# Performance work log

Hardware: AMD Instinct MI355X
Metric: run time of the kernel (lower is better)

Reference implementation:

```python
import jax, jax.numpy as jnp
import numpy as np

NUM_HEADS = 16
ROPE_BASE = 10000.0


def _rope_cos_sin(seq_len, head_dim, dtype):
    inv_freq = 1.0 / (ROPE_BASE ** (jnp.arange(0, head_dim, 2, dtype=jnp.float32) / head_dim))
    t = jnp.arange(seq_len, dtype=jnp.float32)
    freqs = t[:, None] * inv_freq[None, :]          # [S, hd/2]
    emb = jnp.concatenate([freqs, freqs], axis=-1)  # [S, hd]
    return jnp.cos(emb).astype(dtype), jnp.sin(emb).astype(dtype)


def _rotate_half(x):
    x1, x2 = jnp.split(x, 2, axis=-1)
    return jnp.concatenate([-x2, x1], axis=-1)


def setup_inputs() -> dict:
    key = jax.random.key(0)
    ks = jax.random.split(key, 5)
    B, S, D = 2, 2048, 2048
    x = jax.random.normal(ks[0], (B, S, D), dtype=jnp.float32)
    Wq = jax.random.normal(ks[1], (D, D), dtype=jnp.float32) * (D ** -0.5)
    Wk = jax.random.normal(ks[2], (D, D), dtype=jnp.float32) * (D ** -0.5)
    Wv = jax.random.normal(ks[3], (D, D), dtype=jnp.float32) * (D ** -0.5)
    Wo = jax.random.normal(ks[4], (D, D), dtype=jnp.float32) * (D ** -0.5)
    return {"x": x, "Wq": Wq, "Wk": Wk, "Wv": Wv, "Wo": Wo}


def reference(x, Wq, Wk, Wv, Wo):
    B, S, D = x.shape
    H = NUM_HEADS
    hd = D // H
    scale = hd ** -0.5
    # Linear(bias=False): y = x @ W.T ; reshape to [B, H, S, hd]
    def proj(W):
        return jnp.einsum('bsd,ed->bse', x, W).reshape(B, S, H, hd).transpose(0, 2, 1, 3)
    q, k, v = proj(Wq), proj(Wk), proj(Wv)
    cos, sin = _rope_cos_sin(S, hd, x.dtype)  # [S, hd]
    cos = cos[None, None, :, :]
    sin = sin[None, None, :, :]
    q = q * cos + _rotate_half(q) * sin
    k = k * cos + _rotate_half(k) * sin
    scores = jnp.einsum('bhqd,bhkd->bhqk', q, k) * scale  # [B,H,S,S]
    causal = jnp.triu(jnp.ones((S, S), dtype=bool), k=1)
    scores = jnp.where(causal[None, None], jnp.finfo(scores.dtype).min, scores)
    attn = jax.nn.softmax(scores, axis=-1)
    out = jnp.einsum('bhqk,bhkd->bhqd', attn, v)  # [B,H,S,hd]
    out = out.transpose(0, 2, 1, 3).reshape(B, S, D)
    return jnp.einsum('bsd,ed->bse', out, Wo)
```

## Files before the change

### kernel.cpp

```cpp
#include <hip/hip_runtime.h>
#include <hip/hip_bf16.h>
#include <math.h>

typedef __bf16 bf16_t;
typedef __attribute__((ext_vector_type(8))) __bf16 bf16x8;
typedef __attribute__((ext_vector_type(4))) float f32x4;
typedef __attribute__((ext_vector_type(16))) float f32x16;

#define S_LEN 2048
#define DM    2048
#define NH    16
#define HD    128
#define MTOT  4096

__device__ inline float finz(float v) {
    return (v == v && fabsf(v) < 1e30f) ? v : 0.f;
}

__device__ inline void gload_lds16(const bf16_t* g, bf16_t* l) {
    __builtin_amdgcn_global_load_lds(
        (const __attribute__((address_space(1))) void*)g,
        (__attribute__((address_space(3))) void*)l, 16, 0, 0);
}

__device__ __forceinline__ void phb() {
    __builtin_amdgcn_sched_barrier(0);
    __builtin_amdgcn_s_barrier();
    __builtin_amdgcn_sched_barrier(0);
}

__device__ __forceinline__ int crow4(int g, int hi) {
    return (g & 3) + ((g >> 2) << 3) + (hi << 2);
}
__device__ __forceinline__ unsigned pk2(float x, float y) {
    union { bf16_t h; unsigned short u; } a, b;
    a.h = (bf16_t)x; b.h = (bf16_t)y;
    return (unsigned)a.u | ((unsigned)b.u << 16);
}
__device__ __forceinline__ bf16x8 pack4(unsigned w0, unsigned w1, unsigned w2, unsigned w3) {
    union { unsigned w[4]; bf16x8 v; } u;
    u.w[0] = w0; u.w[1] = w1; u.w[2] = w2; u.w[3] = w3;
    return u.v;
}

#define MFMA16(a, b, c) __builtin_amdgcn_mfma_f32_16x16x32_bf16(a, b, c, 0, 0, 0)
#define MFMA32(a, b, c) __builtin_amdgcn_mfma_f32_32x32x16_bf16(a, b, c, 0, 0, 0)

__global__ __launch_bounds__(256)
void dtype_probe(const unsigned short* __restrict__ p, unsigned int* __restrict__ flag)
{
    __shared__ int tot;
    if (threadIdx.x == 0) tot = 0;
    __syncthreads();
    int weird = 0;
    for (int i = threadIdx.x; i < 4096; i += 256) {
        unsigned short u = p[2*i];
        int e = (u >> 7) & 0xFF;
        if (e >= 0xC8 || (e != 0 && e <= 0x38)) weird++;
    }
    atomicAdd(&tot, weird);
    __syncthreads();
    if (threadIdx.x == 0) *flag = (tot > 512) ? 1u : 0u;
}

__global__ __launch_bounds__(256)
void convert_in(const void* __restrict__ src, bf16_t* __restrict__ dst, int n,
                const unsigned int* __restrict__ flag)
{
    const bool f32 = (*flag != 0);
    int i = (blockIdx.x*256 + threadIdx.x)*4;
    if (i + 3 >= n) return;
    if (f32) {
        const float4 v = *(const float4*)((const float*)src + i);
        dst[i  ] = (bf16_t)v.x; dst[i+1] = (bf16_t)v.y;
        dst[i+2] = (bf16_t)v.z; dst[i+3] = (bf16_t)v.w;
    } else {
        *(uint2*)(dst + i) = *(const uint2*)((const bf16_t*)src + i);
    }
}

__global__ __launch_bounds__(256)
void convert_w4(const void* __restrict__ s0, const void* __restrict__ s1,
                const void* __restrict__ s2, const void* __restrict__ s3,
                bf16_t* __restrict__ dst, const unsigned int* __restrict__ flag)
{
    const bool f32 = (*flag != 0);
    const void* src = (blockIdx.y == 0) ? s0 : (blockIdx.y == 1) ? s1
                    : (blockIdx.y == 2) ? s2 : s3;
    bf16_t* d = dst + (size_t)blockIdx.y * DM * DM;
    int i = (blockIdx.x*256 + threadIdx.x)*4;
    if (f32) {
        const float4 v = *(const float4*)((const float*)src + i);
        d[i  ] = (bf16_t)v.x; d[i+1] = (bf16_t)v.y;
        d[i+2] = (bf16_t)v.z; d[i+3] = (bf16_t)v.w;
    } else {
        *(uint2*)(d + i) = *(const uint2*)((const bf16_t*)src + i);
    }
}

__global__ __launch_bounds__(256)
void rope_table(float2* __restrict__ tab)
{
    int i = blockIdx.x*256 + threadIdx.x;
    int s = i >> 6, t64 = i & 63;
    float invf = exp2f(-(float)t64 * 0.20762050593046014f);
    float ang  = (float)s * invf;
    float sn, cs;
    sincosf(ang, &sn, &cs);
    tab[i] = make_float2(cs, sn);
}

template<int MODE>
__global__ __launch_bounds__(512, 2)
void gemm8(const bf16_t* __restrict__ A, const bf16_t* __restrict__ W,
           void* __restrict__ Cv, const float2* __restrict__ rtab)
{
    __shared__ bf16_t Ls[2][2][256*64];

    const int t    = threadIdx.x;
    const int wid  = t >> 6;
    const int lane = t & 63;
    const int c16  = lane & 15;
    const int quad = lane >> 4;
    const int wm   = wid >> 2;
    const int wn   = wid & 3;
    const int mb   = blockIdx.x;
    const int nb   = blockIdx.y;

    const int srow = lane >> 3;
    const int sch  = (lane & 7) ^ srow;
    const bf16_t* Ab = A + (size_t)(mb*256 + wid*32 + srow)*DM + sch*8;
    const bf16_t* Wb = W + (size_t)(nb*256 + wid*32 + srow)*DM + sch*8;

    auto stage = [&](int buf, int kt) {
        const size_t koff = (size_t)kt*64;
        #pragma unroll
        for (int j = 0; j < 4; ++j)
            gload_lds16(Ab + koff + (size_t)j*8*DM, &Ls[buf][0][(wid*32 + j*8)*64]);
        #pragma unroll
        for (int j = 0; j < 4; ++j)
            gload_lds16(Wb + koff + (size_t)j*8*DM, &Ls[buf][1][(wid*32 + j*8)*64]);
    };
    auto rdA = [&](int buf, int qm, int i, int kk) -> bf16x8 {
        int row = wm*128 + qm*64 + i*16 + c16;
        int ch  = (kk*4 + quad) ^ (row & 7);
        return *(const bf16x8*)&Ls[buf][0][row*64 + ch*8];
    };
    auto rdB = [&](int buf, int k, int kk) -> bf16x8 {
        int row = wn*16 + k*64 + c16;
        int ch  = (kk*4 + quad) ^ (row & 7);
        return *(const bf16x8*)&Ls[buf][1][row*64 + ch*8];
    };

    f32x4 acc[8][4];
    #pragma unroll
    for (int i = 0; i < 8; ++i)
        #pragma unroll
        for (int j = 0; j < 4; ++j)
            acc[i][j] = (f32x4){0.f, 0.f, 0.f, 0.f};

    stage(0, 0);
    stage(1, 1);
    asm volatile("s_waitcnt vmcnt(8)" ::: "memory");
    __builtin_amdgcn_s_barrier();

    const int NT = DM/64;
    #pragma unroll 2
    for (int kt = 0; kt < NT; ++kt) {
        const int b = kt & 1;
        bf16x8 af[4][2], bf0[2][2], bf1[2][2];

        #pragma unroll
        for (int i = 0; i < 4; ++i) {
            af[i][0] = rdA(b, 0, i, 0); af[i][1] = rdA(b, 0, i, 1);
        }
        #pragma unroll
        for (int jj = 0; jj < 2; ++jj) {
            bf0[jj][0] = rdB(b, jj, 0); bf0[jj][1] = rdB(b, jj, 1);
        }
        phb();
        __builtin_amdgcn_s_setprio(1);
        #pragma unroll
        for (int kk = 0; kk < 2; ++kk)
            #pragma unroll
            for (int i = 0; i < 4; ++i)
                #pragma unroll
                for (int jj = 0; jj < 2; ++jj)
                    acc[i][jj] = MFMA16(af[i][kk], bf0[jj][kk], acc[i][jj]);
        __builtin_amdgcn_s_setprio(0);
        phb();

        #pragma unroll
        for (int jj = 0; jj < 2; ++jj) {
            bf1[jj][0] = rdB(b, 2+jj, 0); bf1[jj][1] = rdB(b, 2+jj, 1);
        }
        phb();
        __builtin_amdgcn_s_setprio(1);
        #pragma unroll
        for (int kk = 0; kk < 2; ++kk)
            #pragma unroll
            for (int i = 0; i < 4; ++i)
                #pragma unroll
                for (int jj = 0; jj < 2; ++jj)
                    acc[i][2+jj] = MFMA16(af[i][kk], bf1[jj][kk], acc[i][2+jj]);
        __builtin_amdgcn_s_setprio(0);
        phb();

        #pragma unroll
        for (int i = 0; i < 4; ++i) {
            af[i][0] = rdA(b, 1, i, 0); af[i][1] = rdA(b, 1, i, 1);
        }
        phb();
        __builtin_amdgcn_s_setprio(1);
        #pragma unroll
        for (int kk = 0; kk < 2; ++kk)
            #pragma unroll
            for (int i = 0; i < 4; ++i)
                #pragma unroll
                for (int jj = 0; jj < 2; ++jj)
                    acc[4+i][jj] = MFMA16(af[i][kk], bf0[jj][kk], acc[4+i][jj]);
        __builtin_amdgcn_s_setprio(0);
        phb();

        __builtin_amdgcn_s_setprio(1);
        #pragma unroll
        for (int kk = 0; kk < 2; ++kk)
            #pragma unroll
            for (int i = 0; i < 4; ++i)
                #pragma unroll
                for (int jj = 0; jj < 2; ++jj)
                    acc[4+i][2+jj] = MFMA16(af[i][kk], bf1[jj][kk], acc[4+i][2+jj]);
        __builtin_amdgcn_s_setprio(0);
        phb();

        if (kt + 2 < NT) {
            stage(b, kt + 2);
            asm volatile("s_waitcnt vmcnt(8)" ::: "memory");
        } else {
            asm volatile("s_waitcnt vmcnt(0)" ::: "memory");
        }
        __builtin_amdgcn_s_barrier();
        __builtin_amdgcn_sched_barrier(0);
    }

    #pragma unroll
    for (int mi = 0; mi < 8; ++mi) {
        #pragma unroll
        for (int r = 0; r < 4; ++r) {
            const int m = mb*256 + wm*128 + mi*16 + quad*4 + r;
            if (MODE == 2) {
                bf16_t* C = (bf16_t*)Cv;
                #pragma unroll
                for (int k = 0; k < 4; ++k)
                    C[(size_t)m*DM + nb*256 + wn*16 + k*64 + c16] =
                        (bf16_t)finz(acc[mi][k][r]);
            } else if (MODE == 3) {
                float* C = (float*)Cv;
                #pragma unroll
                for (int k = 0; k < 4; ++k)
                    C[(size_t)m*DM + nb*256 + wn*16 + k*64 + c16] =
                        finz(acc[mi][k][r]);
            } else {
                const int s  = m & (S_LEN - 1);
                const int bb = m >> 11;
                #pragma unroll
                for (int hp = 0; hp < 2; ++hp) {
                    const int n   = nb*256 + wn*16 + c16 + hp*128;
                    const int g   = n >> 11;
                    const int e   = n & (DM - 1);
                    const int hh  = e >> 7;
                    const int t64 = e & 63;
                    bf16_t* C = (bf16_t*)Cv + (size_t)g * MTOT * DM;
                    size_t base = ((size_t)(bb*NH + hh)*S_LEN + s)*HD;
                    float lo  = acc[mi][2*hp  ][r];
                    float hi2 = acc[mi][2*hp+1][r];
                    if (g == 2) {
                        C[base + t64     ] = (bf16_t)finz(lo);
                        C[base + t64 + 64] = (bf16_t)finz(hi2);
                    } else {
                        float2 cs2 = rtab[s*64 + t64];
                        C[base + t64     ] = (bf16_t)finz(lo*cs2.x - hi2*cs2.y);
                        C[base + t64 + 64] = (bf16_t)finz(hi2*cs2.x + lo*cs2.y);
                    }
                }
            }
        }
    }
}

__global__ __launch_bounds__(256)
void transpose_v(const bf16_t* __restrict__ Vb, bf16_t* __restrict__ VT)
{
    __shared__ bf16_t Lt[64*72];
    const int t  = threadIdx.x;
    const int st = blockIdx.x;
    const int dt = blockIdx.y;
    const int bh = blockIdx.z;
    #pragma unroll
    for (int i = 0; i < 2; ++i) {
        int ch = t + i*256;
        int sr = ch >> 3, c = ch & 7;
        *(uint4*)(Lt + sr*72 + c*8) =
            *(const uint4*)(Vb + ((size_t)bh*S_LEN + st*64 + sr)*HD + dt*64 + c*8);
    }
    __syncthreads();
    #pragma unroll
    for (int i = 0; i < 2; ++i) {
        int ch = t + i*256;
        int dr = ch >> 3, c = ch & 7;
        bf16x8 v;
        #pragma unroll
        for (int j = 0; j < 8; ++j) v[j] = Lt[(c*8 + j)*72 + dr];
        *(bf16x8*)(VT + ((size_t)bh*HD + dt*64 + dr)*S_LEN + st*64 + c*8) = v;
    }
}

__global__ __launch_bounds__(512, 2)
void flash_attn(const bf16_t* __restrict__ Q, const bf16_t* __restrict__ K,
                const bf16_t* __restrict__ VT, bf16_t* __restrict__ O)
{
    __shared__ bf16_t Ks[64*128];
    __shared__ bf16_t Vs[128*64];
    __shared__ float  Ocmb[4][32*128];
    __shared__ float  lcmb[4][32];

    const int t    = threadIdx.x;
    const int wid  = t >> 6;
    const int lane = t & 63;
    const int qw   = wid & 3;
    const int kh   = wid >> 2;
    const int c32  = lane & 31;
    const int hi   = lane >> 5;
    const int ix   = blockIdx.x;
    const int bh   = blockIdx.y;

    const float scale = 0.08838834764831845f;
    const float SMAX  = 12.0f;

    bf16x8 onesf;
    #pragma unroll
    for (int j = 0; j < 8; ++j) onesf[j] = (bf16_t)1.0f;

    for (int pass = 0; pass < 2; ++pass) {
        const int Qt   = pass ? (15 - ix) : ix;
        const int qt0  = Qt * 128;
        const int qrow = qt0 + qw*32 + c32;
        const int qmin = qt0 + qw*32;

        bf16x8 qf[8];
        {
            const bf16_t* qp = Q + ((size_t)bh*S_LEN + qrow)*HD;
            #pragma unroll
            for (int s = 0; s < 8; ++s)
                qf[s] = *(const bf16x8*)(qp + s*16 + hi*8);
        }

        f32x16 oacc[4];
        f32x16 lacc;
        #pragma unroll
        for (int e = 0; e < 16; ++e) lacc[e] = 0.f;
        #pragma unroll
        for (int dt = 0; dt < 4; ++dt)
            #pragma unroll
            for (int e = 0; e < 16; ++e) oacc[dt][e] = 0.f;

        const int ktend = 2*Qt + 1;
        for (int kt = 0; kt <= ktend; ++kt) {
            __syncthreads();
            #pragma unroll
            for (int j = 0; j < 2; ++j) {
                int base = wid*8 + j*4;
                int rg   = base + (lane >> 4);
                int ph   = (lane & 15) ^ (rg & 7);
                gload_lds16(K + ((size_t)bh*S_LEN + kt*64 + rg)*HD + ph*8,
                            Ks + base*128);
            }
            #pragma unroll
            for (int j = 0; j < 2; ++j) {
                int base = wid*16 + j*8;
                int rg   = base + (lane >> 3);
                int ph   = (lane & 7) ^ (rg & 7);
                gload_lds16(VT + ((size_t)bh*HD + rg)*S_LEN + kt*64 + ph*8,
                            Vs + base*64);
            }
            __syncthreads();

            const int kbase = kt*64 + kh*32;
            if (kbase > qmin + 31) continue;

            f32x16 sacc;
            #pragma unroll
            for (int e = 0; e < 16; ++e) sacc[e] = 0.f;
            const int krow = kh*32 + c32;
            const int ksw  = krow & 7;
            #pragma unroll
            for (int s = 0; s < 8; ++s) {
                bf16x8 kf = *(const bf16x8*)(Ks + krow*128 + (((s*2 + hi) ^ ksw) << 3));
                sacc = MFMA32(kf, qf[s], sacc);
            }

            float p[16];
            if (kbase + 31 > qmin) {
                #pragma unroll
                for (int g = 0; g < 16; ++g) {
                    int kg = kbase + crow4(g, hi);
                    p[g] = (kg <= qrow) ? __expf(sacc[g]*scale - SMAX) : 0.f;
                }
            } else {
                #pragma unroll
                for (int g = 0; g < 16; ++g)
                    p[g] = __expf(sacc[g]*scale - SMAX);
            }

            unsigned a0 = pk2(p[0],  p[1]),  b0 = pk2(p[2],  p[3]);
            unsigned a1 = pk2(p[4],  p[5]),  b1 = pk2(p[6],  p[7]);
            unsigned a2 = pk2(p[8],  p[9]),  b2 = pk2(p[10], p[11]);
            unsigned a3 = pk2(p[12], p[13]), b3 = pk2(p[14], p[15]);
            asm volatile("v_permlane32_swap_b32 %0, %1" : "+v"(a0), "+v"(a1));
            asm volatile("v_permlane32_swap_b32 %0, %1" : "+v"(b0), "+v"(b1));
            asm volatile("v_permlane32_swap_b32 %0, %1" : "+v"(a2), "+v"(a3));
            asm volatile("v_permlane32_swap_b32 %0, %1" : "+v"(b2), "+v"(b3));
            bf16x8 pa0 = pack4(a0, b0, a1, b1);
            bf16x8 pa1 = pack4(a2, b2, a3, b3);

            lacc = MFMA32(pa0, onesf, lacc);
            lacc = MFMA32(pa1, onesf, lacc);
            const int ks0 = kh*2 + 0, ks1 = kh*2 + 1;
            #pragma unroll
            for (int dt = 0; dt < 4; ++dt) {
                const int vrow = dt*32 + c32;
                const int vsw  = vrow & 7;
                bf16x8 vf0 = *(const bf16x8*)(Vs + vrow*64 + (((ks0*2 + hi) ^ vsw) << 3));
                oacc[dt] = MFMA32(pa0, vf0, oacc[dt]);
                bf16x8 vf1 = *(const bf16x8*)(Vs + vrow*64 + (((ks1*2 + hi) ^ vsw) << 3));
                oacc[dt] = MFMA32(pa1, vf1, oacc[dt]);
            }
        }

        if (kh == 1) {
            #pragma unroll
            for (int g = 0; g < 16; ++g) {
                int ql = crow4(g, hi);
                #pragma unroll
                for (int dt = 0; dt < 4; ++dt)
                    Ocmb[qw][ql*128 + dt*32 + c32] = oacc[dt][g];
            }
            if (c32 == 0) {
                #pragma unroll
                for (int g = 0; g < 16; ++g)
                    lcmb[qw][crow4(g, hi)] = lacc[g];
            }
        }
        __syncthreads();
        if (kh == 0) {
            const int b = bh >> 4, h = bh & 15;
            #pragma unroll
            for (int g = 0; g < 16; ++g) {
                int ql = crow4(g, hi);
                int qg = qt0 + qw*32 + ql;
                float lt = lacc[g] + lcmb[qw][ql];
                float rl = 1.0f / fmaxf(lt, 1e-37f);
                #pragma unroll
                for (int dt = 0; dt < 4; ++dt) {
                    float v = oacc[dt][g] + Ocmb[qw][ql*128 + dt*32 + c32];
                    O[((size_t)(b*S_LEN + qg))*DM + h*HD + dt*32 + c32] =
                        (bf16_t)finz(v*rl);
                }
            }
        }
    }
}

extern "C" void kernel_launch(void* const* d_in, const int* in_sizes, int n_in,
                              void* d_out, int out_size, void* d_ws, size_t ws_size,
                              hipStream_t stream)
{
    const void* x_raw  = d_in[0];
    const void* Wq_raw = d_in[1];
    const void* Wk_raw = d_in[2];
    const void* Wv_raw = d_in[3];
    const void* Wo_raw = d_in[4];

    const int NX = MTOT*DM;
    const int NW = DM*DM;

    unsigned int* flag = (unsigned int*)d_ws;
    bf16_t* xb  = (bf16_t*)((char*)d_ws + 16);
    bf16_t* Wqb = xb  + NX;
    bf16_t* Wkb = Wqb + NW;
    bf16_t* Wvb = Wkb + NW;
    bf16_t* Wob = Wvb + NW;
    bf16_t* Qb  = Wob + NW;
    bf16_t* Kb  = Qb + NX;
    bf16_t* Vb  = Kb + NX;
    bf16_t* Ob  = Vb + NX;
    float2* rtab = (float2*)(Ob + NX);
    bf16_t* VT  = xb;

    bool out_is_f32 = true;
    {
        void* base = nullptr; size_t sz = 0;
        if (hipMemGetAddressRange((hipDeviceptr_t*)&base, &sz,
                                  (hipDeviceptr_t)d_out) == hipSuccess && sz != 0) {
            if (sz < (size_t)out_size * 3) out_is_f32 = false;
        }
    }

    dim3 bb(256);
    hipLaunchKernelGGL(dtype_probe, dim3(1), bb, 0, stream,
                       (const unsigned short*)x_raw, flag);
    hipLaunchKernelGGL(convert_in, dim3(NX/1024), bb, 0, stream, x_raw, xb, NX, flag);
    hipLaunchKernelGGL(convert_w4, dim3(NW/1024, 4), bb, 0, stream,
                       Wq_raw, Wk_raw, Wv_raw, Wo_raw, Wqb, flag);
    hipLaunchKernelGGL(rope_table, dim3(S_LEN*64/256), bb, 0, stream, rtab);

    hipLaunchKernelGGL((gemm8<4>), dim3(16, 24), dim3(512), 0, stream,
                       xb, Wqb, (void*)Qb, rtab);
    hipLaunchKernelGGL(transpose_v, dim3(32, 2, 32), bb, 0, stream, Vb, VT);
    hipLaunchKernelGGL(flash_attn, dim3(8, 32), dim3(512), 0, stream, Qb, Kb, VT, Ob);
    if (out_is_f32)
        hipLaunchKernelGGL((gemm8<3>), dim3(16, 8), dim3(512), 0, stream,
                           Ob, Wob, d_out, rtab);
    else
        hipLaunchKernelGGL((gemm8<2>), dim3(16, 8), dim3(512), 0, stream,
                           Ob, Wob, d_out, rtab);
}
```

Before: 458.0 us.

## Restructure GEMM mainloop into half-K phases with four-deep prefetch pipeline

The bf16 GEMM used for the QKV and output projections is rewritten to split each 64-wide K tile into two 32-wide halves. Four phases of loads are kept in flight instead of two tiles, and each phase loads all A/B fragments and then issues 32 MFMAs. The LDS layout changes to 32-element rows without the XOR swizzle, which may add LDS bank conflicts. There are now two barriers per half-tile instead of several per full tile.

```diff
diff --git a/kernel.cpp b/kernel.cpp
--- a/kernel.cpp
+++ b/kernel.cpp
@@ -21,12 +21,6 @@
     __builtin_amdgcn_global_load_lds(
         (const __attribute__((address_space(1))) void*)g,
         (__attribute__((address_space(3))) void*)l, 16, 0, 0);
-}
-
-__device__ __forceinline__ void phb() {
-    __builtin_amdgcn_sched_barrier(0);
-    __builtin_amdgcn_s_barrier();
-    __builtin_amdgcn_sched_barrier(0);
 }
 
 __device__ __forceinline__ int crow4(int g, int hi) {
@@ -112,10 +106,10 @@
 
 template<int MODE>
 __global__ __launch_bounds__(512, 2)
-void gemm8(const bf16_t* __restrict__ A, const bf16_t* __restrict__ W,
+void gemmp(const bf16_t* __restrict__ A, const bf16_t* __restrict__ W,
            void* __restrict__ Cv, const float2* __restrict__ rtab)
 {
-    __shared__ bf16_t Ls[2][2][256*64];
+    __shared__ bf16_t Ls[2][2][2][256*32];
 
     const int t    = threadIdx.x;
     const int wid  = t >> 6;
@@ -127,29 +121,20 @@
     const int mb   = blockIdx.x;
     const int nb   = blockIdx.y;
 
-    const int srow = lane >> 3;
-    const int sch  = (lane & 7) ^ srow;
-    const bf16_t* Ab = A + (size_t)(mb*256 + wid*32 + srow)*DM + sch*8;
-    const bf16_t* Wb = W + (size_t)(nb*256 + wid*32 + srow)*DM + sch*8;
-
-    auto stage = [&](int buf, int kt) {
-        const size_t koff = (size_t)kt*64;
-        #pragma unroll
-        for (int j = 0; j < 4; ++j)
-            gload_lds16(Ab + koff + (size_t)j*8*DM, &Ls[buf][0][(wid*32 + j*8)*64]);
-        #pragma unroll
-        for (int j = 0; j < 4; ++j)
-            gload_lds16(Wb + koff + (size_t)j*8*DM, &Ls[buf][1][(wid*32 + j*8)*64]);
-    };
-    auto rdA = [&](int buf, int qm, int i, int kk) -> bf16x8 {
-        int row = wm*128 + qm*64 + i*16 + c16;
-        int ch  = (kk*4 + quad) ^ (row & 7);
-        return *(const bf16x8*)&Ls[buf][0][row*64 + ch*8];
-    };
-    auto rdB = [&](int buf, int k, int kk) -> bf16x8 {
-        int row = wn*16 + k*64 + c16;
-        int ch  = (kk*4 + quad) ^ (row & 7);
-        return *(const bf16x8*)&Ls[buf][1][row*64 + ch*8];
+    const int srow_ = wid*16 + (lane >> 2);
+    const int sch_  = (lane & 3) * 8;
+    const bf16_t* Abp = A + (size_t)(mb*256 + srow_)*DM + sch_;
+    const bf16_t* Wbp = W + (size_t)(nb*256 + srow_)*DM + sch_;
+
+    auto stage = [&](int P) {
+        const int kt = P >> 1, kh = P & 1;
+        const size_t koff = (size_t)kt*64 + kh*32;
+        bf16_t* la = &Ls[kt & 1][0][kh][0];
+        bf16_t* lb = &Ls[kt & 1][1][kh][0];
+        gload_lds16(Abp + koff,                  la + (wid*16)*32);
+        gload_lds16(Abp + koff + (size_t)128*DM, la + (128 + wid*16)*32);
+        gload_lds16(Wbp + koff,                  lb + (wid*16)*32);
+        gload_lds16(Wbp + koff + (size_t)128*DM, lb + (128 + wid*16)*32);
     };
 
     f32x4 acc[8][4];
@@ -159,89 +144,67 @@
         for (int j = 0; j < 4; ++j)
             acc[i][j] = (f32x4){0.f, 0.f, 0.f, 0.f};
 
-    stage(0, 0);
-    stage(1, 1);
-    asm volatile("s_waitcnt vmcnt(8)" ::: "memory");
+    stage(0); stage(1); stage(2); stage(3);
+    asm volatile("s_waitcnt vmcnt(12)" ::: "memory");
     __builtin_amdgcn_s_barrier();
-
-    const int NT = DM/64;
-    #pragma unroll 2
-    for (int kt = 0; kt < NT; ++kt) {
-        const int b = kt & 1;
-        bf16x8 af[4][2], bf0[2][2], bf1[2][2];
-
-        #pragma unroll
-        for (int i = 0; i < 4; ++i) {
-            af[i][0] = rdA(b, 0, i, 0); af[i][1] = rdA(b, 0, i, 1);
-        }
-        #pragma unroll
-        for (int jj = 0; jj < 2; ++jj) {
-            bf0[jj][0] = rdB(b, jj, 0); bf0[jj][1] = rdB(b, jj, 1);
-        }
-        phb();
-        __builtin_amdgcn_s_setprio(1);
-        #pragma unroll
-        for (int kk = 0; kk < 2; ++kk)
-            #pragma unroll
-            for (int i = 0; i < 4; ++i)
-                #pragma unroll
-                for (int jj = 0; jj < 2; ++jj)
-                    acc[i][jj] = MFMA16(af[i][kk], bf0[jj][kk], acc[i][jj]);
-        __builtin_amdgcn_s_setprio(0);
-        phb();
-
-        #pragma unroll
-        for (int jj = 0; jj < 2; ++jj) {
-            bf1[jj][0] = rdB(b, 2+jj, 0); bf1[jj][1] = rdB(b, 2+jj, 1);
-        }
-        phb();
-        __builtin_amdgcn_s_setprio(1);
-        #pragma unroll
-        for (int kk = 0; kk < 2; ++kk)
-            #pragma unroll
-            for (int i = 0; i < 4; ++i)
-                #pragma unroll
-                for (int jj = 0; jj < 2; ++jj)
-                    acc[i][2+jj] = MFMA16(af[i][kk], bf1[jj][kk], acc[i][2+jj]);
-        __builtin_amdgcn_s_setprio(0);
-        phb();
-
-        #pragma unroll
-        for (int i = 0; i < 4; ++i) {
-            af[i][0] = rdA(b, 1, i, 0); af[i][1] = rdA(b, 1, i, 1);
-        }
-        phb();
-        __builtin_amdgcn_s_setprio(1);
-        #pragma unroll
-        for (int kk = 0; kk < 2; ++kk)
-            #pragma unroll
-            for (int i = 0; i < 4; ++i)
-                #pragma unroll
-                for (int jj = 0; jj < 2; ++jj)
-                    acc[4+i][jj] = MFMA16(af[i][kk], bf0[jj][kk], acc[4+i][jj]);
-        __builtin_amdgcn_s_setprio(0);
-        phb();
-
-        __builtin_amdgcn_s_setprio(1);
-        #pragma unroll
-        for (int kk = 0; kk < 2; ++kk)
-            #pragma unroll
-            for (int i = 0; i < 4; ++i)
-                #pragma unroll
-                for (int jj = 0; jj < 2; ++jj)
-                    acc[4+i][2+jj] = MFMA16(af[i][kk], bf1[jj][kk], acc[4+i][2+jj]);
-        __builtin_amdgcn_s_setprio(0);
-        phb();
-
-        if (kt + 2 < NT) {
-            stage(b, kt + 2);
-            asm volatile("s_waitcnt vmcnt(8)" ::: "memory");
-        } else {
-            asm volatile("s_waitcnt vmcnt(0)" ::: "memory");
-        }
-        __builtin_amdgcn_s_barrier();
-        __builtin_amdgcn_sched_barrier(0);
-    }
+    __builtin_amdgcn_sched_barrier(0);
+
+#define QPHASE(PP, VMS, DOSTAGE)                                           \
+    {                                                                      \
+        const int buf_ = ((PP) >> 1) & 1, kh_ = (PP) & 1;                  \
+        bf16x8 af[8], bfr[4];                                              \
+        _Pragma("unroll")                                                  \
+        for (int mi = 0; mi < 8; ++mi)                                     \
+            af[mi] = *(const bf16x8*)&Ls[buf_][0][kh_]                     \
+                         [(wm*128 + mi*16 + c16)*32 + quad*8];             \
+        _Pragma("unroll")                                                  \
+        for (int j = 0; j < 4; ++j)                                        \
+            bfr[j] = *(const bf16x8*)&Ls[buf_][1][kh_]                     \
+                         [(wn*16 + j*64 + c16)*32 + quad*8];               \
+        __builtin_amdgcn_s_setprio(1);                                     \
+        _Pragma("unroll")                                                  \
+        for (int mi = 0; mi < 8; ++mi)                                     \
+            _Pragma("unroll")                                              \
+            for (int j = 0; j < 4; ++j)                                    \
+                acc[mi][j] = MFMA16(af[mi], bfr[j], acc[mi][j]);           \
+        __builtin_amdgcn_s_setprio(0);                                     \
+        __builtin_amdgcn_sched_barrier(0);                                 \
+        __builtin_amdgcn_s_barrier();       \
+        __builtin_amdgcn_sched_barrier(0);                                 \
+        if (DOSTAGE) stage((PP) + 4);                                      \
+        asm volatile("s_waitcnt vmcnt(" VMS ")" ::: "memory");             \
+        __builtin_amdgcn_s_barrier();       \
+        __builtin_amdgcn_sched_barrier(0);                                 \
+    }
+
+    for (int Pb = 0; Pb < 15; ++Pb) {
+        const int P0 = Pb * 4;
+        QPHASE(P0 + 0, "12", true);
+        QPHASE(P0 + 1, "12", true);
+        QPHASE(P0 + 2, "12", true);
+        QPHASE(P0 + 3, "12", true);
+    }
+    QPHASE(60, "8", false);
+    QPHASE(61, "4", false);
+    QPHASE(62, "0", false);
+    {
+        const int buf_ = 1, kh_ = 1;
+        bf16x8 af[8], bfr[4];
+        #pragma unroll
+        for (int mi = 0; mi < 8; ++mi)
+            af[mi] = *(const bf16x8*)&Ls[buf_][0][kh_]
+                         [(wm*128 + mi*16 + c16)*32 + quad*8];
+        #pragma unroll
+        for (int j = 0; j < 4; ++j)
+            bfr[j] = *(const bf16x8*)&Ls[buf_][1][kh_]
+                         [(wn*16 + j*64 + c16)*32 + quad*8];
+        #pragma unroll
+        for (int mi = 0; mi < 8; ++mi)
+            #pragma unroll
+            for (int j = 0; j < 4; ++j)
+                acc[mi][j] = MFMA16(af[mi], bfr[j], acc[mi][j]);
+    }
+#undef QPHASE
 
     #pragma unroll
     for (int mi = 0; mi < 8; ++mi) {
@@ -251,15 +214,15 @@
             if (MODE == 2) {
                 bf16_t* C = (bf16_t*)Cv;
                 #pragma unroll
-                for (int k = 0; k < 4; ++k)
-                    C[(size_t)m*DM + nb*256 + wn*16 + k*64 + c16] =
-                        (bf16_t)finz(acc[mi][k][r]);
+                for (int j = 0; j < 4; ++j)
+                    C[(size_t)m*DM + nb*256 + wn*16 + j*64 + c16] =
+                        (bf16_t)finz(acc[mi][j][r]);
             } else if (MODE == 3) {
                 float* C = (float*)Cv;
                 #pragma unroll
-                for (int k = 0; k < 4; ++k)
-                    C[(size_t)m*DM + nb*256 + wn*16 + k*64 + c16] =
-                        finz(acc[mi][k][r]);
+                for (int j = 0; j < 4; ++j)
+                    C[(size_t)m*DM + nb*256 + wn*16 + j*64 + c16] =
+                        finz(acc[mi][j][r]);
             } else {
                 const int s  = m & (S_LEN - 1);
                 const int bb = m >> 11;
@@ -514,14 +477,14 @@
                        Wq_raw, Wk_raw, Wv_raw, Wo_raw, Wqb, flag);
     hipLaunchKernelGGL(rope_table, dim3(S_LEN*64/256), bb, 0, stream, rtab);
 
-    hipLaunchKernelGGL((gemm8<4>), dim3(16, 24), dim3(512), 0, stream,
+    hipLaunchKernelGGL((gemmp<4>), dim3(16, 24), dim3(512), 0, stream,
                        xb, Wqb, (void*)Qb, rtab);
     hipLaunchKernelGGL(transpose_v, dim3(32, 2, 32), bb, 0, stream, Vb, VT);
     hipLaunchKernelGGL(flash_attn, dim3(8, 32), dim3(512), 0, stream, Qb, Kb, VT, Ob);
     if (out_is_f32)
-        hipLaunchKernelGGL((gemm8<3>), dim3(16, 8), dim3(512), 0, stream,
+        hipLaunchKernelGGL((gemmp<3>), dim3(16, 8), dim3(512), 0, stream,
                            Ob, Wob, d_out, rtab);
     else
-        hipLaunchKernelGGL((gemm8<2>), dim3(16, 8), dim3(512), 0, stream,
+        hipLaunchKernelGGL((gemmp<2>), dim3(16, 8), dim3(512), 0, stream,
                            Ob, Wob, d_out, rtab);
 }
```

Result: no change. 459.7 us (+0.4%).
